# Kernel optimization log

Measured on AMD Instinct MI355X. Metric: run time of the kernel, lower is better.

The kernel has to match this reference:

```python
import jax, jax.numpy as jnp
import numpy as np

D = 1024
H = 16
HD = D // H
MLP = 4 * D
EPS = 1e-5


def layernorm(x, g, b):
    mu = jnp.mean(x, axis=-1, keepdims=True)
    var = jnp.mean(jnp.square(x - mu), axis=-1, keepdims=True)
    return (x - mu) * jax.lax.rsqrt(var + EPS) * g + b


def setup_inputs() -> dict:
    key = jax.random.key(0)
    ks = jax.random.split(key, 12)
    s = 0.02
    return {
        "x": jax.random.normal(ks[0], (2, 2048, D), jnp.float32),
        "ln1_g": jnp.ones((D,), jnp.float32),
        "ln1_b": jnp.zeros((D,), jnp.float32),
        "lnm_g": jnp.ones((D,), jnp.float32),
        "lnm_b": jnp.zeros((D,), jnp.float32),
        "qkv_w": jax.random.normal(ks[1], (D, 3 * D), jnp.float32) * s,
        "qkv_b": jnp.zeros((3 * D,), jnp.float32),
        "proj_w": jax.random.normal(ks[2], (D, D), jnp.float32) * s,
        "proj_b": jnp.zeros((D,), jnp.float32),
        "fc1_w": jax.random.normal(ks[3], (D, MLP), jnp.float32) * s,
        "fc1_b": jnp.zeros((MLP,), jnp.float32),
        "fc2_w": jax.random.normal(ks[4], (MLP, D), jnp.float32) * s,
        "fc2_b": jnp.zeros((D,), jnp.float32),
    }


def reference(x, ln1_g, ln1_b, lnm_g, lnm_b, qkv_w, qkv_b, proj_w, proj_b,
              fc1_w, fc1_b, fc2_w, fc2_b):
    B, N, _ = x.shape
    scale = HD ** -0.5
    # --- self-attention on norm1(x) ---
    h = layernorm(x, ln1_g, ln1_b)
    qkv = h @ qkv_w + qkv_b                       # [B, N, 3D]
    qkv = qkv.reshape(B, N, 3, H, HD)
    q, k, v = qkv[:, :, 0], qkv[:, :, 1], qkv[:, :, 2]  # [B, N, H, HD]
    attn = jnp.einsum("bqhd,bkhd->bhqk", q, k) * scale
    attn = jax.nn.softmax(attn, axis=-1)
    o = jnp.einsum("bhqk,bkhd->bqhd", attn, v).reshape(B, N, D)
    x = x + (o @ proj_w + proj_b)
    # --- MLP ---
    m = layernorm(x, lnm_g, lnm_b)
    m = jax.nn.gelu(m @ fc1_w + fc1_b, approximate=False)
    x = x + (m @ fc2_w + fc2_b)
    return x
```

## Files before the change

### kernel.cpp

```cpp
#include <hip/hip_runtime.h>

typedef __bf16 bf16_t;
typedef bf16_t bf16x4 __attribute__((ext_vector_type(4)));
typedef bf16_t bf16x8 __attribute__((ext_vector_type(8)));
typedef float f32x4 __attribute__((ext_vector_type(4)));
typedef unsigned short u16x8 __attribute__((ext_vector_type(8)));

#define MFMA(a, b, c) __builtin_amdgcn_mfma_f32_16x16x32_bf16(a, b, c, 0, 0, 0)

__device__ inline float exp2_fast(float x) {
  float r;
  asm volatile("v_exp_f32 %0, %1" : "=v"(r) : "v"(x));
  return r;
}

__device__ inline void gll16(const bf16_t* g, bf16_t* l) {
  __builtin_amdgcn_global_load_lds(
      (const __attribute__((address_space(1))) unsigned int*)(g),
      (__attribute__((address_space(3))) unsigned int*)(l), 16, 0, 0);
}

__device__ inline float gelu_f(float v) {
  float ax = fabsf(v) * 0.70710678118f;
  float t = __builtin_amdgcn_rcpf(1.0f + 0.3275911f * ax);
  float p = ((((1.061405429f * t - 1.453152027f) * t + 1.421413741f) * t -
              0.284496736f) * t + 0.254829592f) * t;
  float e = exp2_fast(-ax * ax * 1.4426950408889634f);
  float erf = 1.0f - p * e;
  erf = v < 0.f ? -erf : erf;
  return 0.5f * v * (1.0f + erf);
}

__global__ __launch_bounds__(256) void ln_kernel(const float* __restrict__ x,
                                                 const float* __restrict__ g,
                                                 const float* __restrict__ b,
                                                 bf16_t* __restrict__ out) {
  long row = blockIdx.x;
  const float4* xr = (const float4*)(x + row * 1024);
  float4 v = xr[threadIdx.x];
  float s = v.x + v.y + v.z + v.w;
  float s2 = v.x * v.x + v.y * v.y + v.z * v.z + v.w * v.w;
#pragma unroll
  for (int m = 32; m >= 1; m >>= 1) {
    s += __shfl_xor(s, m);
    s2 += __shfl_xor(s2, m);
  }
  __shared__ float red[8];
  int wid = threadIdx.x >> 6;
  if ((threadIdx.x & 63) == 0) {
    red[wid] = s;
    red[4 + wid] = s2;
  }
  __syncthreads();
  s = red[0] + red[1] + red[2] + red[3];
  s2 = red[4] + red[5] + red[6] + red[7];
  float mu = s * (1.f / 1024.f);
  float rs = rsqrtf(s2 * (1.f / 1024.f) - mu * mu + 1e-5f);
  float4 gv = ((const float4*)g)[threadIdx.x];
  float4 bv = ((const float4*)b)[threadIdx.x];
  bf16_t o0 = (bf16_t)((v.x - mu) * rs * gv.x + bv.x);
  bf16_t o1 = (bf16_t)((v.y - mu) * rs * gv.y + bv.y);
  bf16_t o2 = (bf16_t)((v.z - mu) * rs * gv.z + bv.z);
  bf16_t o3 = (bf16_t)((v.w - mu) * rs * gv.w + bv.w);
  ushort4 pk;
  pk.x = *(unsigned short*)&o0;
  pk.y = *(unsigned short*)&o1;
  pk.z = *(unsigned short*)&o2;
  pk.w = *(unsigned short*)&o3;
  *(ushort4*)(out + row * 1024 + threadIdx.x * 4) = pk;
}

__global__ void wconv_kernel(const float* __restrict__ W, bf16_t* __restrict__ Wt,
                             int K, int N) {
  __shared__ float t[32][33];
  int n0 = blockIdx.x * 32, k0 = blockIdx.y * 32;
#pragma unroll
  for (int s = 0; s < 4; s++) {
    int k = threadIdx.y + s * 8;
    t[k][threadIdx.x] = W[(long)(k0 + k) * N + n0 + threadIdx.x];
  }
  __syncthreads();
#pragma unroll
  for (int s = 0; s < 4; s++) {
    int n = threadIdx.y + s * 8;
    Wt[(long)(n0 + n) * K + k0 + threadIdx.x] = (bf16_t)t[threadIdx.x][n];
  }
}

#define STAGE_PTR(DA, DB, k0)                 \
  gll16(ga + (k0), DA + w * 512);             \
  gll16(ga + (k0) + astep, DA + 4096 + w * 512); \
  gll16(gb + (k0), DB + w * 512);

#define COMPUTE(LA, LB)                                                \
  {                                                                    \
    bf16x8 af[4], bfr[4];                                              \
    _Pragma("unroll") for (int mt = 0; mt < 4; mt++) af[mt] =          \
        *(const bf16x8*)(LA + (wm + mt * 16 + l15) * 32 + quad * 8);   \
    _Pragma("unroll") for (int nt = 0; nt < 4; nt++) bfr[nt] =         \
        *(const bf16x8*)(LB + (wn + nt * 16 + l15) * 32 + quad * 8);   \
    _Pragma("unroll") for (int mt = 0; mt < 4; mt++)                   \
        _Pragma("unroll") for (int nt = 0; nt < 4; nt++) acc[mt][nt] = \
            MFMA(af[mt], bfr[nt], acc[mt][nt]);                        \
  }

#define WB3 asm volatile("s_waitcnt vmcnt(3)\ns_barrier" ::: "memory")
#define WB0 asm volatile("s_waitcnt vmcnt(0)\ns_barrier" ::: "memory")

__global__ __launch_bounds__(512, 4) void gemm_kernel(
    const bf16_t* __restrict__ A, const bf16_t* __restrict__ Bt,
    const float* __restrict__ bias, const float* __restrict__ resid,
    void* __restrict__ Cout, int M, int N, int K, int epi) {
  __shared__ bf16_t lA0[256 * 32], lB0[128 * 32];
  __shared__ bf16_t lA1[256 * 32], lB1[128 * 32];
  __shared__ bf16_t lA2[256 * 32], lB2[128 * 32];
  int tid = threadIdx.x;
  int bn = blockIdx.x, bm = blockIdx.y;
  int kchunk = K / gridDim.z;
  int kbeg = blockIdx.z * kchunk, kend = kbeg + kchunk;

  int lane = tid & 63, w = tid >> 6;
  int quad = lane >> 4, l15 = lane & 15;
  int wm = (w & 3) * 64, wn = (w >> 2) * 64;

  f32x4 acc[4][4];
#pragma unroll
  for (int i = 0; i < 4; i++)
#pragma unroll
    for (int j = 0; j < 4; j++) acc[i][j] = (f32x4){0.f, 0.f, 0.f, 0.f};

  const bf16_t* ga = A + (long)(bm * 256 + w * 16 + (lane >> 2)) * K + (lane & 3) * 8;
  const bf16_t* gb = Bt + (long)(bn * 128 + w * 16 + (lane >> 2)) * K + (lane & 3) * 8;
  long astep = (long)128 * K;

  int nit = (kend - kbeg) >> 5;
  bf16_t *A0 = lA0, *A1 = lA1, *A2 = lA2;
  bf16_t *B0 = lB0, *B1 = lB1, *B2 = lB2;
  STAGE_PTR(A0, B0, kbeg);
  STAGE_PTR(A1, B1, kbeg + 32);
  for (int i = 0; i < nit; i++) {
    if (i + 1 < nit) { WB3; } else { WB0; }
    if (i + 2 < nit) {
      int ks = kbeg + (i + 2) * 32;
      STAGE_PTR(A2, B2, ks);
    }
    COMPUTE(A0, B0);
    bf16_t* t;
    t = A0; A0 = A1; A1 = A2; A2 = t;
    t = B0; B0 = B1; B1 = B2; B2 = t;
  }

#pragma unroll
  for (int mt = 0; mt < 4; mt++) {
#pragma unroll
    for (int r = 0; r < 4; r++) {
      long row = bm * 256 + wm + mt * 16 + quad * 4 + r;
#pragma unroll
      for (int nt = 0; nt < 4; nt++) {
        int col = bn * 128 + wn + nt * 16 + l15;
        long idx = row * N + col;
        if (epi == 3) {
          ((bf16_t*)Cout)[(long)blockIdx.z * M * N + idx] = (bf16_t)acc[mt][nt][r];
        } else {
          float v = acc[mt][nt][r] + bias[col];
          if (epi == 1) {
            ((float*)Cout)[idx] = v + resid[idx];
          } else if (epi == 2) {
            ((bf16_t*)Cout)[idx] = (bf16_t)gelu_f(v);
          } else {
            ((bf16_t*)Cout)[idx] = (bf16_t)v;
          }
        }
      }
    }
  }
}

__global__ __launch_bounds__(256) void reduce_ln_kernel(
    const bf16_t* __restrict__ p, const float* __restrict__ bias,
    const float* __restrict__ resid, float* __restrict__ x1,
    const float* __restrict__ g, const float* __restrict__ bb,
    bf16_t* __restrict__ mb) {
  const long MN = (long)4096 * 1024;
  long row = blockIdx.x;
  int t = threadIdx.x;
  bf16x4 a0 = *(const bf16x4*)(p + row * 1024 + t * 4);
  bf16x4 a1 = *(const bf16x4*)(p + MN + row * 1024 + t * 4);
  bf16x4 a2 = *(const bf16x4*)(p + 2 * MN + row * 1024 + t * 4);
  bf16x4 a3 = *(const bf16x4*)(p + 3 * MN + row * 1024 + t * 4);
  float4 r = ((const float4*)(resid + row * 1024))[t];
  float4 bv = ((const float4*)bias)[t];
  float4 v;
  v.x = (float)a0[0] + (float)a1[0] + (float)a2[0] + (float)a3[0] + r.x + bv.x;
  v.y = (float)a0[1] + (float)a1[1] + (float)a2[1] + (float)a3[1] + r.y + bv.y;
  v.z = (float)a0[2] + (float)a1[2] + (float)a2[2] + (float)a3[2] + r.z + bv.z;
  v.w = (float)a0[3] + (float)a1[3] + (float)a2[3] + (float)a3[3] + r.w + bv.w;
  ((float4*)(x1 + row * 1024))[t] = v;
  float s = v.x + v.y + v.z + v.w;
  float s2 = v.x * v.x + v.y * v.y + v.z * v.z + v.w * v.w;
#pragma unroll
  for (int m = 32; m >= 1; m >>= 1) {
    s += __shfl_xor(s, m);
    s2 += __shfl_xor(s2, m);
  }
  __shared__ float red[8];
  int wid = t >> 6;
  if ((t & 63) == 0) {
    red[wid] = s;
    red[4 + wid] = s2;
  }
  __syncthreads();
  s = red[0] + red[1] + red[2] + red[3];
  s2 = red[4] + red[5] + red[6] + red[7];
  float mu = s * (1.f / 1024.f);
  float rs = rsqrtf(s2 * (1.f / 1024.f) - mu * mu + 1e-5f);
  float4 gv = ((const float4*)g)[t];
  float4 b2 = ((const float4*)bb)[t];
  bf16_t o0 = (bf16_t)((v.x - mu) * rs * gv.x + b2.x);
  bf16_t o1 = (bf16_t)((v.y - mu) * rs * gv.y + b2.y);
  bf16_t o2 = (bf16_t)((v.z - mu) * rs * gv.z + b2.z);
  bf16_t o3 = (bf16_t)((v.w - mu) * rs * gv.w + b2.w);
  ushort4 pk;
  pk.x = *(unsigned short*)&o0;
  pk.y = *(unsigned short*)&o1;
  pk.z = *(unsigned short*)&o2;
  pk.w = *(unsigned short*)&o3;
  *(ushort4*)(mb + row * 1024 + t * 4) = pk;
}

__global__ __launch_bounds__(256) void reduce4_kernel(const bf16_t* __restrict__ p,
                                                      const float* __restrict__ bias,
                                                      const float* __restrict__ resid,
                                                      float* __restrict__ out) {
  long i = (long)blockIdx.x * 256 + threadIdx.x;
  const long MN = (long)4096 * 1024;
  bf16x4 a0 = *(const bf16x4*)(p + i * 4);
  bf16x4 a1 = *(const bf16x4*)(p + MN + i * 4);
  bf16x4 a2 = *(const bf16x4*)(p + 2 * MN + i * 4);
  bf16x4 a3 = *(const bf16x4*)(p + 3 * MN + i * 4);
  float4 r = ((const float4*)resid)[i];
  float4 bv = ((const float4*)bias)[i & 255];
  float4 o;
  o.x = (float)a0[0] + (float)a1[0] + (float)a2[0] + (float)a3[0] + r.x + bv.x;
  o.y = (float)a0[1] + (float)a1[1] + (float)a2[1] + (float)a3[1] + r.y + bv.y;
  o.z = (float)a0[2] + (float)a1[2] + (float)a2[2] + (float)a3[2] + r.z + bv.z;
  o.w = (float)a0[3] + (float)a1[3] + (float)a2[3] + (float)a3[3] + r.w + bv.w;
  ((float4*)out)[i] = o;
}

#define LDV 72

__global__ __launch_bounds__(256) void attn_kernel(const bf16_t* __restrict__ qkv,
                                                   bf16_t* __restrict__ o) {
  const int LD = 3072;
  int flat = blockIdx.x;
  int slot = flat >> 3;
  int bh = (flat & 7) * 4 + (slot >> 5);
  int qt = slot & 31;
  int h = bh & 15, b = bh >> 4;

  int tid = threadIdx.x, w = tid >> 6, lane = tid & 63;
  int quad = lane >> 4, l15 = lane & 15;
  int qrow = qt * 64 + w * 16;
  const bf16_t* base = qkv + (long)b * 2048 * LD + h * 64;
  const bf16_t* Qp = base;
  const bf16_t* Kp = base + 1024;
  const bf16_t* Vp = base + 2048;

  __shared__ bf16_t lK[64 * 64];
  __shared__ bf16_t lV[64 * LDV];
  __shared__ bf16_t lP[4][16 * LDV];
  bf16_t* myp = lP[w];

  const bf16_t* kg =
      Kp + (long)(w * 16 + (lane >> 3)) * LD + (((lane & 7) ^ (lane >> 3)) & 7) * 8;
  bf16_t* lkd = lK + w * 1024;
  int kk = tid & 31;
  int d0 = (tid >> 5) * 8;
  const bf16_t* vg = Vp + (long)(2 * kk) * LD + d0;
  unsigned int* lvw = (unsigned int*)lV;

  bf16x8 qf[2];
#pragma unroll
  for (int d = 0; d < 2; d++)
    qf[d] = *(const bf16x8*)(Qp + (long)(qrow + l15) * LD + d * 32 + quad * 8);

  f32x4 oacc[4];
#pragma unroll
  for (int t = 0; t < 4; t++) oacc[t] = (f32x4){0.f, 0.f, 0.f, 0.f};
  float li_p[4] = {0.f, 0.f, 0.f, 0.f};
  const float c2 = 0.18033688011112042f;

  int sw0 = (quad ^ l15) & 7;
  int sw1 = ((quad + 4) ^ l15) & 7;

  for (int kt = 0; kt < 2048; kt += 64) {
    long koff = (long)kt * LD;
    u16x8 va = *(const u16x8*)(vg + koff);
    u16x8 vb = *(const u16x8*)(vg + koff + LD);
    __syncthreads();
    gll16(kg + koff, lkd);
    gll16(kg + koff + 8 * (long)LD, lkd + 512);
#pragma unroll
    for (int j = 0; j < 8; j++)
      lvw[(d0 + j) * (LDV / 2) + kk] = (unsigned int)va[j] | ((unsigned int)vb[j] << 16);
    __syncthreads();

    f32x4 s[4];
#pragma unroll
    for (int st = 0; st < 4; st++) {
      const bf16_t* krow = lK + (st * 16 + l15) * 64;
      f32x4 z = (f32x4){0.f, 0.f, 0.f, 0.f};
      z = MFMA(qf[0], *(const bf16x8*)(krow + sw0 * 8), z);
      s[st] = MFMA(qf[1], *(const bf16x8*)(krow + sw1 * 8), z);
    }

#pragma unroll
    for (int st = 0; st < 4; st++)
#pragma unroll
      for (int r = 0; r < 4; r++) {
        float p = exp2_fast(s[st][r] * c2);
        s[st][r] = p;
        li_p[r] += p;
      }

#pragma unroll
    for (int r = 0; r < 4; r++)
#pragma unroll
      for (int st = 0; st < 4; st++)
        myp[(quad * 4 + r) * LDV + st * 16 + l15] = (bf16_t)s[st][r];
    asm volatile("s_waitcnt lgkmcnt(0)" ::: "memory");

    bf16x8 pa0 = *(const bf16x8*)(myp + l15 * LDV + quad * 8);
    bf16x8 pa1 = *(const bf16x8*)(myp + l15 * LDV + 32 + quad * 8);
#pragma unroll
    for (int t = 0; t < 4; t++) {
      const bf16_t* vr = lV + (t * 16 + l15) * LDV + quad * 8;
      oacc[t] = MFMA(pa0, *(const bf16x8*)(vr), oacc[t]);
      oacc[t] = MFMA(pa1, *(const bf16x8*)(vr + 32), oacc[t]);
    }
  }

  float li[4];
#pragma unroll
  for (int r = 0; r < 4; r++) {
    float s = li_p[r];
#pragma unroll
    for (int x = 8; x >= 1; x >>= 1) s += __shfl_xor(s, x);
    li[r] = s;
  }
#pragma unroll
  for (int t = 0; t < 4; t++)
#pragma unroll
    for (int r = 0; r < 4; r++) {
      long q = qrow + quad * 4 + r;
      o[((long)b * 2048 + q) * 1024 + h * 64 + t * 16 + l15] =
          (bf16_t)(oacc[t][r] / li[r]);
    }
}

extern "C" void kernel_launch(void* const* d_in, const int* in_sizes, int n_in,
                              void* d_out, int out_size, void* d_ws, size_t ws_size,
                              hipStream_t stream) {
  (void)in_sizes; (void)n_in; (void)out_size; (void)ws_size;
  const float* x = (const float*)d_in[0];
  const float* ln1_g = (const float*)d_in[1];
  const float* ln1_b = (const float*)d_in[2];
  const float* lnm_g = (const float*)d_in[3];
  const float* lnm_b = (const float*)d_in[4];
  const float* qkv_w = (const float*)d_in[5];
  const float* qkv_b = (const float*)d_in[6];
  const float* proj_w = (const float*)d_in[7];
  const float* proj_b = (const float*)d_in[8];
  const float* fc1_w = (const float*)d_in[9];
  const float* fc1_b = (const float*)d_in[10];
  const float* fc2_w = (const float*)d_in[11];
  const float* fc2_b = (const float*)d_in[12];
  float* out = (float*)d_out;

  const int M = 4096;
  const int D_ = 1024, MLP_ = 4096, QKV = 3072;

  char* ws = (char*)d_ws;
  bf16_t* h = (bf16_t*)(ws);
  bf16_t* qkvb = (bf16_t*)(ws + (8u << 20));
  bf16_t* ob = (bf16_t*)(ws + (32u << 20));
  float* x1 = (float*)(ws + (40u << 20));
  bf16_t* mb = (bf16_t*)(ws + (56u << 20));
  bf16_t* gb = (bf16_t*)(ws + (64u << 20));
  bf16_t* qkv_wt = (bf16_t*)(ws + (96u << 20));
  bf16_t* proj_wt = (bf16_t*)(ws + (102u << 20));
  bf16_t* fc1_wt = (bf16_t*)(ws + (104u << 20));
  bf16_t* fc2_wt = (bf16_t*)(ws + (112u << 20));
  bf16_t* p_proj = (bf16_t*)(ws);
  bf16_t* p_fc2 = (bf16_t*)(ws);

  dim3 tb(32, 8);
  wconv_kernel<<<dim3(QKV / 32, D_ / 32), tb, 0, stream>>>(qkv_w, qkv_wt, D_, QKV);
  wconv_kernel<<<dim3(D_ / 32, D_ / 32), tb, 0, stream>>>(proj_w, proj_wt, D_, D_);
  wconv_kernel<<<dim3(MLP_ / 32, D_ / 32), tb, 0, stream>>>(fc1_w, fc1_wt, D_, MLP_);
  wconv_kernel<<<dim3(D_ / 32, MLP_ / 32), tb, 0, stream>>>(fc2_w, fc2_wt, MLP_, D_);

  ln_kernel<<<M, 256, 0, stream>>>(x, ln1_g, ln1_b, h);
  gemm_kernel<<<dim3(QKV / 128, M / 256), 512, 0, stream>>>(h, qkv_wt, qkv_b, nullptr,
                                                            qkvb, M, QKV, D_, 0);
  attn_kernel<<<1024, 256, 0, stream>>>(qkvb, ob);
  gemm_kernel<<<dim3(D_ / 128, M / 256, 4), 512, 0, stream>>>(ob, proj_wt, nullptr,
                                                              nullptr, p_proj, M, D_,
                                                              D_, 3);
  reduce_ln_kernel<<<M, 256, 0, stream>>>(p_proj, proj_b, x, x1, lnm_g, lnm_b, mb);
  gemm_kernel<<<dim3(MLP_ / 128, M / 256), 512, 0, stream>>>(mb, fc1_wt, fc1_b,
                                                             nullptr, gb, M, MLP_, D_,
                                                             2);
  gemm_kernel<<<dim3(D_ / 128, M / 256, 4), 512, 0, stream>>>(gb, fc2_wt, nullptr,
                                                              nullptr, p_fc2, M, D_,
                                                              MLP_, 3);
  reduce4_kernel<<<4096, 256, 0, stream>>>(p_fc2, fc2_b, x1, out);
}
```

Before: 405.1 us.

## Process two query tiles per attention warp and vectorize weight conversion

Each attention warp now handles 32 query rows instead of 16, so every K and V fragment loaded from LDS feeds two sets of MFMAs. The grid is halved to 512 blocks and the block-to-(head, query-tile) mapping drops the earlier interleaved swizzle. The weight transpose/convert kernel now uses 64x64 tiles, reads with float4 and writes packed 4-element bf16 vectors, cutting memory transactions. In exchange, attention uses more registers and LDS and launches half as many blocks, which may lower occupancy and change L2 locality.

```diff
diff --git a/kernel.cpp b/kernel.cpp
--- a/kernel.cpp
+++ b/kernel.cpp
@@ -70,21 +70,38 @@
   *(ushort4*)(out + row * 1024 + threadIdx.x * 4) = pk;
 }
 
-__global__ void wconv_kernel(const float* __restrict__ W, bf16_t* __restrict__ Wt,
-                             int K, int N) {
-  __shared__ float t[32][33];
-  int n0 = blockIdx.x * 32, k0 = blockIdx.y * 32;
+__global__ __launch_bounds__(256) void wconv_kernel(const float* __restrict__ W,
+                                                    bf16_t* __restrict__ Wt, int K,
+                                                    int N) {
+  __shared__ float t[64][65];
+  int n0 = blockIdx.x * 64, k0 = blockIdx.y * 64;
+  int tid = threadIdx.x;
+  int c4 = tid & 15;
+  int r = tid >> 4;
 #pragma unroll
   for (int s = 0; s < 4; s++) {
-    int k = threadIdx.y + s * 8;
-    t[k][threadIdx.x] = W[(long)(k0 + k) * N + n0 + threadIdx.x];
+    int k = r + s * 16;
+    float4 v = *(const float4*)(W + (long)(k0 + k) * N + n0 + c4 * 4);
+    t[k][c4 * 4] = v.x;
+    t[k][c4 * 4 + 1] = v.y;
+    t[k][c4 * 4 + 2] = v.z;
+    t[k][c4 * 4 + 3] = v.w;
   }
   __syncthreads();
-#pragma unroll
-  for (int s = 0; s < 4; s++) {
-    int n = threadIdx.y + s * 8;
-    Wt[(long)(n0 + n) * K + k0 + threadIdx.x] = (bf16_t)t[threadIdx.x][n];
-  }
+  int n = tid >> 2;
+  int kc = (tid & 3) * 16;
+  ushort4 pk[4];
+#pragma unroll
+  for (int c = 0; c < 4; c++) {
+#pragma unroll
+    for (int j = 0; j < 4; j++) {
+      bf16_t x = (bf16_t)t[kc + c * 4 + j][n];
+      ((unsigned short*)&pk[c])[j] = *(unsigned short*)&x;
+    }
+  }
+  bf16_t* dst = Wt + (long)(n0 + n) * K + k0 + kc;
+#pragma unroll
+  for (int c = 0; c < 4; c++) *(ushort4*)(dst + c * 4) = pk[c];
 }
 
 #define STAGE_PTR(DA, DB, k0)                 \
@@ -254,14 +271,13 @@
                                                    bf16_t* __restrict__ o) {
   const int LD = 3072;
   int flat = blockIdx.x;
-  int slot = flat >> 3;
-  int bh = (flat & 7) * 4 + (slot >> 5);
-  int qt = slot & 31;
+  int bh = flat >> 4;
+  int qt = flat & 15;
   int h = bh & 15, b = bh >> 4;
 
   int tid = threadIdx.x, w = tid >> 6, lane = tid & 63;
   int quad = lane >> 4, l15 = lane & 15;
-  int qrow = qt * 64 + w * 16;
+  int qrow = qt * 128 + w * 32;
   const bf16_t* base = qkv + (long)b * 2048 * LD + h * 64;
   const bf16_t* Qp = base;
   const bf16_t* Kp = base + 1024;
@@ -269,7 +285,7 @@
 
   __shared__ bf16_t lK[64 * 64];
   __shared__ bf16_t lV[64 * LDV];
-  __shared__ bf16_t lP[4][16 * LDV];
+  __shared__ bf16_t lP[4][32 * LDV];
   bf16_t* myp = lP[w];
 
   const bf16_t* kg =
@@ -280,15 +296,20 @@
   const bf16_t* vg = Vp + (long)(2 * kk) * LD + d0;
   unsigned int* lvw = (unsigned int*)lV;
 
-  bf16x8 qf[2];
-#pragma unroll
-  for (int d = 0; d < 2; d++)
-    qf[d] = *(const bf16x8*)(Qp + (long)(qrow + l15) * LD + d * 32 + quad * 8);
-
-  f32x4 oacc[4];
-#pragma unroll
-  for (int t = 0; t < 4; t++) oacc[t] = (f32x4){0.f, 0.f, 0.f, 0.f};
-  float li_p[4] = {0.f, 0.f, 0.f, 0.f};
+  bf16x8 qf[2][2];
+#pragma unroll
+  for (int qi = 0; qi < 2; qi++)
+#pragma unroll
+    for (int d = 0; d < 2; d++)
+      qf[qi][d] =
+          *(const bf16x8*)(Qp + (long)(qrow + qi * 16 + l15) * LD + d * 32 + quad * 8);
+
+  f32x4 oacc[2][4];
+#pragma unroll
+  for (int qi = 0; qi < 2; qi++)
+#pragma unroll
+    for (int t = 0; t < 4; t++) oacc[qi][t] = (f32x4){0.f, 0.f, 0.f, 0.f};
+  float li_p[2][4] = {{0.f, 0.f, 0.f, 0.f}, {0.f, 0.f, 0.f, 0.f}};
   const float c2 = 0.18033688011112042f;
 
   int sw0 = (quad ^ l15) & 7;
@@ -306,57 +327,81 @@
       lvw[(d0 + j) * (LDV / 2) + kk] = (unsigned int)va[j] | ((unsigned int)vb[j] << 16);
     __syncthreads();
 
-    f32x4 s[4];
+    bf16x8 kf[4][2];
 #pragma unroll
     for (int st = 0; st < 4; st++) {
       const bf16_t* krow = lK + (st * 16 + l15) * 64;
-      f32x4 z = (f32x4){0.f, 0.f, 0.f, 0.f};
-      z = MFMA(qf[0], *(const bf16x8*)(krow + sw0 * 8), z);
-      s[st] = MFMA(qf[1], *(const bf16x8*)(krow + sw1 * 8), z);
-    }
-
-#pragma unroll
-    for (int st = 0; st < 4; st++)
-#pragma unroll
-      for (int r = 0; r < 4; r++) {
-        float p = exp2_fast(s[st][r] * c2);
-        s[st][r] = p;
-        li_p[r] += p;
+      kf[st][0] = *(const bf16x8*)(krow + sw0 * 8);
+      kf[st][1] = *(const bf16x8*)(krow + sw1 * 8);
+    }
+    f32x4 s[2][4];
+#pragma unroll
+    for (int qi = 0; qi < 2; qi++)
+#pragma unroll
+      for (int st = 0; st < 4; st++) {
+        f32x4 z = (f32x4){0.f, 0.f, 0.f, 0.f};
+        z = MFMA(qf[qi][0], kf[st][0], z);
+        s[qi][st] = MFMA(qf[qi][1], kf[st][1], z);
       }
 
 #pragma unroll
-    for (int r = 0; r < 4; r++)
+    for (int qi = 0; qi < 2; qi++)
 #pragma unroll
       for (int st = 0; st < 4; st++)
-        myp[(quad * 4 + r) * LDV + st * 16 + l15] = (bf16_t)s[st][r];
+#pragma unroll
+        for (int r = 0; r < 4; r++) {
+          float p = exp2_fast(s[qi][st][r] * c2);
+          s[qi][st][r] = p;
+          li_p[qi][r] += p;
+        }
+
+#pragma unroll
+    for (int qi = 0; qi < 2; qi++)
+#pragma unroll
+      for (int r = 0; r < 4; r++)
+#pragma unroll
+        for (int st = 0; st < 4; st++)
+          myp[(qi * 16 + quad * 4 + r) * LDV + st * 16 + l15] = (bf16_t)s[qi][st][r];
     asm volatile("s_waitcnt lgkmcnt(0)" ::: "memory");
 
-    bf16x8 pa0 = *(const bf16x8*)(myp + l15 * LDV + quad * 8);
-    bf16x8 pa1 = *(const bf16x8*)(myp + l15 * LDV + 32 + quad * 8);
+    bf16x8 pa[2][2];
+#pragma unroll
+    for (int qi = 0; qi < 2; qi++) {
+      pa[qi][0] = *(const bf16x8*)(myp + (qi * 16 + l15) * LDV + quad * 8);
+      pa[qi][1] = *(const bf16x8*)(myp + (qi * 16 + l15) * LDV + 32 + quad * 8);
+    }
 #pragma unroll
     for (int t = 0; t < 4; t++) {
       const bf16_t* vr = lV + (t * 16 + l15) * LDV + quad * 8;
-      oacc[t] = MFMA(pa0, *(const bf16x8*)(vr), oacc[t]);
-      oacc[t] = MFMA(pa1, *(const bf16x8*)(vr + 32), oacc[t]);
-    }
-  }
-
-  float li[4];
-#pragma unroll
-  for (int r = 0; r < 4; r++) {
-    float s = li_p[r];
-#pragma unroll
-    for (int x = 8; x >= 1; x >>= 1) s += __shfl_xor(s, x);
-    li[r] = s;
-  }
-#pragma unroll
-  for (int t = 0; t < 4; t++)
+      bf16x8 v0 = *(const bf16x8*)(vr);
+      bf16x8 v1 = *(const bf16x8*)(vr + 32);
+#pragma unroll
+      for (int qi = 0; qi < 2; qi++) {
+        oacc[qi][t] = MFMA(pa[qi][0], v0, oacc[qi][t]);
+        oacc[qi][t] = MFMA(pa[qi][1], v1, oacc[qi][t]);
+      }
+    }
+  }
+
+#pragma unroll
+  for (int qi = 0; qi < 2; qi++) {
+    float li[4];
 #pragma unroll
     for (int r = 0; r < 4; r++) {
-      long q = qrow + quad * 4 + r;
-      o[((long)b * 2048 + q) * 1024 + h * 64 + t * 16 + l15] =
-          (bf16_t)(oacc[t][r] / li[r]);
-    }
+      float s = li_p[qi][r];
+#pragma unroll
+      for (int x = 8; x >= 1; x >>= 1) s += __shfl_xor(s, x);
+      li[r] = s;
+    }
+#pragma unroll
+    for (int t = 0; t < 4; t++)
+#pragma unroll
+      for (int r = 0; r < 4; r++) {
+        long q = qrow + qi * 16 + quad * 4 + r;
+        o[((long)b * 2048 + q) * 1024 + h * 64 + t * 16 + l15] =
+            (bf16_t)(oacc[qi][t][r] / li[r]);
+      }
+  }
 }
 
 extern "C" void kernel_launch(void* const* d_in, const int* in_sizes, int n_in,
@@ -395,16 +440,15 @@
   bf16_t* p_proj = (bf16_t*)(ws);
   bf16_t* p_fc2 = (bf16_t*)(ws);
 
-  dim3 tb(32, 8);
-  wconv_kernel<<<dim3(QKV / 32, D_ / 32), tb, 0, stream>>>(qkv_w, qkv_wt, D_, QKV);
-  wconv_kernel<<<dim3(D_ / 32, D_ / 32), tb, 0, stream>>>(proj_w, proj_wt, D_, D_);
-  wconv_kernel<<<dim3(MLP_ / 32, D_ / 32), tb, 0, stream>>>(fc1_w, fc1_wt, D_, MLP_);
-  wconv_kernel<<<dim3(D_ / 32, MLP_ / 32), tb, 0, stream>>>(fc2_w, fc2_wt, MLP_, D_);
+  wconv_kernel<<<dim3(QKV / 64, D_ / 64), 256, 0, stream>>>(qkv_w, qkv_wt, D_, QKV);
+  wconv_kernel<<<dim3(D_ / 64, D_ / 64), 256, 0, stream>>>(proj_w, proj_wt, D_, D_);
+  wconv_kernel<<<dim3(MLP_ / 64, D_ / 64), 256, 0, stream>>>(fc1_w, fc1_wt, D_, MLP_);
+  wconv_kernel<<<dim3(D_ / 64, MLP_ / 64), 256, 0, stream>>>(fc2_w, fc2_wt, MLP_, D_);
 
   ln_kernel<<<M, 256, 0, stream>>>(x, ln1_g, ln1_b, h);
   gemm_kernel<<<dim3(QKV / 128, M / 256), 512, 0, stream>>>(h, qkv_wt, qkv_b, nullptr,
                                                             qkvb, M, QKV, D_, 0);
-  attn_kernel<<<1024, 256, 0, stream>>>(qkvb, ob);
+  attn_kernel<<<512, 256, 0, stream>>>(qkvb, ob);
   gemm_kernel<<<dim3(D_ / 128, M / 256, 4), 512, 0, stream>>>(ob, proj_wt, nullptr,
                                                               nullptr, p_proj, M, D_,
                                                               D_, 3);
```

New measurement: 400.6 us. No clear change (-1.1%).
